# Optimization experiments

Measured on AMD Instinct MI355X. Metric: run time of the kernel, lower is better.

Reference implementation:

```python
import jax, jax.numpy as jnp
import numpy as np

N_HEAD = 4
EPS = 1e-5

def _layernorm(x, g, b):
    mu = jnp.mean(x, axis=-1, keepdims=True)
    var = jnp.mean(jnp.square(x - mu), axis=-1, keepdims=True)
    return (x - mu) * jax.lax.rsqrt(var + EPS) * g + b

def setup_inputs() -> dict:
    key = jax.random.key(0)
    ks = jax.random.split(key, 16)
    B, T, F = 8, 1024, 256
    dk = F // N_HEAD
    s = 1.0 / np.sqrt(F)
    return {
        "x": jax.random.normal(ks[0], (B, T, F), jnp.float32),
        "q_in": jax.random.normal(ks[1], (B, T, F), jnp.float32),
        "pos_k": jax.random.normal(ks[2], (T, T, dk), jnp.float32),
        "mask": jax.random.randint(ks[3], (B, T, T), 0, 2, jnp.int32),
        "ln_g": jnp.ones((F,), jnp.float32),
        "ln_b": jnp.zeros((F,), jnp.float32),
        "Wq": jax.random.normal(ks[4], (F, F), jnp.float32) * s,
        "bq": jnp.zeros((F,), jnp.float32),
        "Wk": jax.random.normal(ks[5], (F, F), jnp.float32) * s,
        "bk": jnp.zeros((F,), jnp.float32),
        "Wv": jax.random.normal(ks[6], (F, F), jnp.float32) * s,
        "bv": jnp.zeros((F,), jnp.float32),
        "Wo": jax.random.normal(ks[7], (F, F), jnp.float32) * s,
        "bo": jnp.zeros((F,), jnp.float32),
    }

def reference(x, q_in, pos_k, mask, ln_g, ln_b, Wq, bq, Wk, bk, Wv, bv, Wo, bo):
    B, T2, F = x.shape
    T1 = q_in.shape[1]
    h = N_HEAD
    dk = F // h
    xn = _layernorm(x, ln_g, ln_b)
    # (B, T, h, dk) -> (B, h, T, dk)
    q = (q_in @ Wq + bq).reshape(B, T1, h, dk).transpose(0, 2, 1, 3)
    k = (xn @ Wk + bk).reshape(B, T2, h, dk).transpose(0, 2, 1, 3)
    v = (xn @ Wv + bv).reshape(B, T2, h, dk).transpose(0, 2, 1, 3)
    A = jnp.einsum('bhqd,bhkd->bhqk', q, k)
    # relative position bias: B[b,h,q,t] = sum_d q[b,h,q,d] * pos_k[q,t,d]
    Bmat = jnp.einsum('bhqd,qtd->bhqt', q, pos_k)
    scores = (A + Bmat) / np.sqrt(dk)
    m = (mask[:, None, :, :] == 0)  # (B,1,T1,T2)
    min_val = jnp.finfo(scores.dtype).min
    scores = jnp.where(m, min_val, scores)
    attn = jax.nn.softmax(scores, axis=-1)
    attn = jnp.where(m, 0.0, attn)
    out = jnp.einsum('bhqk,bhkd->bhqd', attn, v)
    out = out.transpose(0, 2, 1, 3).reshape(B, T1, F)
    return out @ Wo + bo
```

## Files before the change

### kernel.cpp

```cpp
#include <hip/hip_runtime.h>
#include <hip/hip_bf16.h>

#define TT 1024
#define FF 256

typedef float  f4v  __attribute__((ext_vector_type(4)));
typedef float  f16v __attribute__((ext_vector_type(16)));
typedef __bf16 bf8v __attribute__((ext_vector_type(8)));
typedef unsigned short us8v __attribute__((ext_vector_type(8)));
typedef unsigned short us4v __attribute__((ext_vector_type(4)));

static __device__ __forceinline__ unsigned short f2bf(float x) {
    return __builtin_bit_cast(unsigned short, (__bf16)x);
}
static __device__ __forceinline__ float bf2f(unsigned short u) {
    return (float)__builtin_bit_cast(__bf16, u);
}
static __device__ __forceinline__ bf8v us2bf(us8v v) {
    return __builtin_bit_cast(bf8v, v);
}

__global__ __launch_bounds__(256) void k_wprep(
    const float* __restrict__ Wq, const float* __restrict__ Wk,
    const float* __restrict__ Wv, const float* __restrict__ Wo,
    unsigned short* __restrict__ Wt)
{
    __shared__ unsigned short T[32][36];
    const float* W = (blockIdx.y == 0) ? Wq : (blockIdx.y == 1) ? Wk
                   : (blockIdx.y == 2) ? Wv : Wo;
    unsigned short* dst = Wt + (blockIdx.y << 16);
    const int kt = (blockIdx.x >> 3) << 5, nt = (blockIdx.x & 7) << 5;
    const int r = threadIdx.x >> 3, c0 = (threadIdx.x & 7) << 2;
    const f4v w = *(const f4v*)&W[(kt + r) * FF + nt + c0];
    #pragma unroll
    for (int j = 0; j < 4; ++j) T[c0 + j][r] = f2bf(w[j]);
    __syncthreads();
    *(us4v*)&dst[(nt + r) * FF + kt + c0] = *(const us4v*)&T[r][c0];
}

__global__ __launch_bounds__(256) void k_ln(
    const float* __restrict__ x, const float* __restrict__ qin,
    const float* __restrict__ lng, const float* __restrict__ lnb,
    unsigned short* __restrict__ xn_bf, unsigned short* __restrict__ qin_bf)
{
    const int tid = threadIdx.x, lane = tid & 63, wv = tid >> 6;
    const int r0 = blockIdx.x << 4;

    #pragma unroll
    for (int u = 0; u < 4; ++u) {
        const int i4 = ((u << 8) + tid) << 2;
        const int r = i4 >> 8, c = i4 & 255;
        const f4v qv = *(const f4v*)&qin[(r0 + r) * FF + c];
        us4v o;
        #pragma unroll
        for (int j = 0; j < 4; ++j) o[j] = f2bf(qv[j]);
        *(us4v*)&qin_bf[(r0 + r) * FF + c] = o;
    }

    #pragma unroll
    for (int rr = 0; rr < 4; ++rr) {
        const int row = r0 + (wv << 2) + rr;
        float v[4], s = 0.f, s2 = 0.f;
        #pragma unroll
        for (int c4 = 0; c4 < 4; ++c4) {
            v[c4] = x[row * FF + (c4 << 6) + lane];
            s += v[c4]; s2 += v[c4] * v[c4];
        }
        #pragma unroll
        for (int off = 1; off < 64; off <<= 1) {
            s  += __shfl_xor(s, off);
            s2 += __shfl_xor(s2, off);
        }
        const float mu  = s * (1.f / FF);
        const float rsd = rsqrtf(s2 * (1.f / FF) - mu * mu + 1e-5f);
        #pragma unroll
        for (int c4 = 0; c4 < 4; ++c4) {
            const int c = (c4 << 6) + lane;
            xn_bf[row * FF + c] = f2bf((v[c4] - mu) * rsd * lng[c] + lnb[c]);
        }
    }
}

__global__ __launch_bounds__(256) void k_proj(
    const unsigned short* __restrict__ qin_bf, const unsigned short* __restrict__ xn_bf,
    const unsigned short* __restrict__ Wt,
    const float* __restrict__ bq, const float* __restrict__ bk, const float* __restrict__ bv,
    unsigned short* __restrict__ Qh, unsigned short* __restrict__ Kh,
    unsigned short* __restrict__ Vt)
{
    __shared__ __align__(16) unsigned short As[64 * 264];
    const int z = blockIdx.y;
    const unsigned short* A = (z == 0) ? qin_bf : xn_bf;
    const unsigned short* W = Wt + (z << 16);
    const float* bias = (z == 0) ? bq : (z == 1) ? bk : bv;
    unsigned short* dst = (z == 0) ? Qh : (z == 1) ? Kh : Vt;
    const int tid = threadIdx.x;
    const int m0 = blockIdx.x << 6;

    #pragma unroll
    for (int u = 0; u < 8; ++u) {
        const int idx = (u << 8) + tid;
        const int r = idx >> 5, c = (idx & 31) << 3;
        *(us8v*)&As[r * 264 + c] = *(const us8v*)&A[(m0 + r) * FF + c];
    }
    __syncthreads();

    const int lane = tid & 63, nw = tid >> 6, gq = lane >> 5, l31 = lane & 31;
    f16v acc[2][2];
    #pragma unroll
    for (int i = 0; i < 2; ++i)
        #pragma unroll
        for (int j = 0; j < 2; ++j)
            #pragma unroll
            for (int e = 0; e < 16; ++e) acc[i][j][e] = 0.f;

    for (int ks = 0; ks < 16; ++ks) {
        const int k0 = (ks << 4) + (gq << 3);
        bf8v af[2], wf[2];
        af[0] = us2bf(*(const us8v*)&As[l31 * 264 + k0]);
        af[1] = us2bf(*(const us8v*)&As[(32 + l31) * 264 + k0]);
        wf[0] = us2bf(*(const us8v*)&W[((nw << 6) + l31) * FF + k0]);
        wf[1] = us2bf(*(const us8v*)&W[((nw << 6) + 32 + l31) * FF + k0]);
        if (z == 2) {
            #pragma unroll
            for (int ti = 0; ti < 2; ++ti)
                #pragma unroll
                for (int tj = 0; tj < 2; ++tj)
                    acc[ti][tj] = __builtin_amdgcn_mfma_f32_32x32x16_bf16(
                        wf[tj], af[ti], acc[ti][tj], 0, 0, 0);
        } else {
            #pragma unroll
            for (int ti = 0; ti < 2; ++ti)
                #pragma unroll
                for (int tj = 0; tj < 2; ++tj)
                    acc[ti][tj] = __builtin_amdgcn_mfma_f32_32x32x16_bf16(
                        af[ti], wf[tj], acc[ti][tj], 0, 0, 0);
        }
    }

    if (z != 2) {
        #pragma unroll
        for (int ti = 0; ti < 2; ++ti)
            #pragma unroll
            for (int tj = 0; tj < 2; ++tj)
                #pragma unroll
                for (int reg = 0; reg < 16; ++reg) {
                    const int row = (reg & 3) + ((reg >> 2) << 3) + (gq << 2);
                    const int tg = m0 + (ti << 5) + row;
                    const int n = (nw << 6) + (tj << 5) + l31;
                    float val = acc[ti][tj][reg] + bias[n];
                    if (z == 0) val *= 0.125f;
                    const int b = tg >> 10, t = tg & 1023;
                    dst[(((b << 2) + nw) << 16) + (t << 6) + (tj << 5) + l31] = f2bf(val);
                }
    } else {
        #pragma unroll
        for (int ti = 0; ti < 2; ++ti)
            #pragma unroll
            for (int tj = 0; tj < 2; ++tj)
                #pragma unroll
                for (int reg = 0; reg < 16; ++reg) {
                    const int row = (reg & 3) + ((reg >> 2) << 3) + (gq << 2);
                    const int d = (tj << 5) + row;
                    const int tg = m0 + (ti << 5) + l31;
                    const float val = acc[ti][tj][reg] + bias[(nw << 6) + d];
                    const int b = tg >> 10, t = tg & 1023;
                    dst[(((b << 2) + nw) << 16) + (d << 10) + t] = f2bf(val);
                }
    }
}

__global__ __launch_bounds__(256) void k_bterm(
    const unsigned short* __restrict__ Qh, const float* __restrict__ posk,
    const int* __restrict__ mask, unsigned short* __restrict__ Bm, int qbase)
{
    const int tid = threadIdx.x, lane = tid & 63, wv = tid >> 6;
    const int gq = lane >> 5, m = lane & 31;
    const int ql = blockIdx.y, q = qbase + ql;

    bf8v afr[4];
    #pragma unroll
    for (int kk = 0; kk < 4; ++kk)
        afr[kk] = us2bf(*(const us8v*)&Qh[(m << 16) + (q << 6) + (kk << 4) + (gq << 3)]);

    const int t0w = (blockIdx.x << 9) + (wv << 7);
    for (int st = 0; st < 4; ++st) {
        const int t = t0w + (st << 5) + m;
        bf8v bfr[4];
        #pragma unroll
        for (int kk = 0; kk < 4; ++kk) {
            const int d0 = (kk << 4) + (gq << 3);
            const f4v p0 = *(const f4v*)&posk[(((q << 10) + t) << 6) + d0];
            const f4v p1 = *(const f4v*)&posk[(((q << 10) + t) << 6) + d0 + 4];
            bf8v bb;
            bb[0] = (__bf16)p0[0]; bb[1] = (__bf16)p0[1];
            bb[2] = (__bf16)p0[2]; bb[3] = (__bf16)p0[3];
            bb[4] = (__bf16)p1[0]; bb[5] = (__bf16)p1[1];
            bb[6] = (__bf16)p1[2]; bb[7] = (__bf16)p1[3];
            bfr[kk] = bb;
        }
        f16v acc;
        #pragma unroll
        for (int i = 0; i < 16; ++i) acc[i] = 0.f;
        #pragma unroll
        for (int kk = 0; kk < 4; ++kk)
            acc = __builtin_amdgcn_mfma_f32_32x32x16_bf16(afr[kk], bfr[kk], acc, 0, 0, 0);

        int mk[4];
        #pragma unroll
        for (int g = 0; g < 4; ++g)
            mk[g] = mask[(((g << 1) + gq) << 20) + (q << 10) + t];
        #pragma unroll
        for (int reg = 0; reg < 16; ++reg) {
            const int g = reg >> 2;
            const int bhr = (reg & 3) + (g << 3) + (gq << 2);
            const float val = mk[g] ? acc[reg] : -3.0e38f;
            Bm[(bhr << 19) + (ql << 10) + t] = f2bf(val);
        }
    }
}

__global__ __launch_bounds__(256) void k_attn(
    const unsigned short* __restrict__ Qh, const unsigned short* __restrict__ Kh,
    const unsigned short* __restrict__ Vt, const unsigned short* __restrict__ Bm,
    unsigned short* __restrict__ aout_bf, int qbase)
{
    __shared__ __align__(16) unsigned short Qs[32 * 72];
    __shared__ __align__(16) unsigned short Ps[32 * 136];
    __shared__ __align__(16) unsigned short Bs[32 * 136];
    __shared__ float m_s[32], l_s[32], wmax[4][32], wsum[4][32];

    const int tid = threadIdx.x, lane = tid & 63, wv = tid >> 6;
    const int l15 = lane & 15, quad = lane >> 4;
    const int bh = blockIdx.x & 31, qt = blockIdx.x >> 5;
    const int b = bh >> 2, h = bh & 3;
    const int q0l = qt << 5, q0g = qbase + q0l;

    if (tid < 32) { m_s[tid] = -3.0e38f; l_s[tid] = 0.f; }
    {
        const int r = tid >> 3, d0 = (tid & 7) << 3;
        *(us8v*)&Qs[r * 72 + d0] =
            *(const us8v*)&Qh[(bh << 16) + ((q0g + r) << 6) + d0];
    }

    f4v o0, o1;
    #pragma unroll
    for (int i = 0; i < 4; ++i) { o0[i] = 0.f; o1[i] = 0.f; }

    for (int it = 0; it < 8; ++it) {
        const int t0 = it << 7;
        #pragma unroll
        for (int u = 0; u < 2; ++u) {
            const int idx = (u << 8) + tid;
            const int r = idx >> 4, c = (idx & 15) << 3;
            *(us8v*)&Bs[r * 136 + c] =
                *(const us8v*)&Bm[(bh << 19) + ((q0l + r) << 10) + t0 + c];
        }
        __syncthreads();

        f4v s00, s01, s10, s11;
        #pragma unroll
        for (int i = 0; i < 4; ++i) { s00[i]=0.f; s01[i]=0.f; s10[i]=0.f; s11[i]=0.f; }
        #pragma unroll
        for (int kk = 0; kk < 2; ++kk) {
            const int d0 = (kk << 5) + (quad << 3);
            const bf8v aq0 = us2bf(*(const us8v*)&Qs[l15 * 72 + d0]);
            const bf8v aq1 = us2bf(*(const us8v*)&Qs[(16 + l15) * 72 + d0]);
            const bf8v kb0 = us2bf(*(const us8v*)&Kh[(bh << 16) + ((t0 + (wv << 5) + l15) << 6) + d0]);
            const bf8v kb1 = us2bf(*(const us8v*)&Kh[(bh << 16) + ((t0 + (wv << 5) + 16 + l15) << 6) + d0]);
            s00 = __builtin_amdgcn_mfma_f32_16x16x32_bf16(aq0, kb0, s00, 0, 0, 0);
            s01 = __builtin_amdgcn_mfma_f32_16x16x32_bf16(aq0, kb1, s01, 0, 0, 0);
            s10 = __builtin_amdgcn_mfma_f32_16x16x32_bf16(aq1, kb0, s10, 0, 0, 0);
            s11 = __builtin_amdgcn_mfma_f32_16x16x32_bf16(aq1, kb1, s11, 0, 0, 0);
        }

        float sv[2][2][4];
        #pragma unroll
        for (int mf = 0; mf < 2; ++mf)
            #pragma unroll
            for (int nf = 0; nf < 2; ++nf) {
                const f4v sfr = (mf == 0) ? (nf == 0 ? s00 : s01)
                                          : (nf == 0 ? s10 : s11);
                const int tl = (wv << 5) + (nf << 4) + l15;
                #pragma unroll
                for (int r = 0; r < 4; ++r) {
                    const int q = (mf << 4) + (quad << 2) + r;
                    sv[mf][nf][r] = sfr[r] + bf2f(Bs[q * 136 + tl]);
                }
            }

        float rmax[2][4];
        #pragma unroll
        for (int mf = 0; mf < 2; ++mf)
            #pragma unroll
            for (int r = 0; r < 4; ++r) {
                float vx = fmaxf(sv[mf][0][r], sv[mf][1][r]);
                vx = fmaxf(vx, __shfl_xor(vx, 1));
                vx = fmaxf(vx, __shfl_xor(vx, 2));
                vx = fmaxf(vx, __shfl_xor(vx, 4));
                vx = fmaxf(vx, __shfl_xor(vx, 8));
                rmax[mf][r] = vx;
            }
        if (l15 == 0) {
            #pragma unroll
            for (int mf = 0; mf < 2; ++mf)
                #pragma unroll
                for (int r = 0; r < 4; ++r)
                    wmax[wv][(mf << 4) + (quad << 2) + r] = rmax[mf][r];
        }
        __syncthreads();

        float alpha[2][4], mnew[2][4];
        #pragma unroll
        for (int mf = 0; mf < 2; ++mf)
            #pragma unroll
            for (int r = 0; r < 4; ++r) {
                const int q = (mf << 4) + (quad << 2) + r;
                const float tm = fmaxf(fmaxf(wmax[0][q], wmax[1][q]),
                                       fmaxf(wmax[2][q], wmax[3][q]));
                const float mo = m_s[q];
                const float mn = fmaxf(mo, tm);
                mnew[mf][r]  = mn;
                alpha[mf][r] = __expf(mo - mn);
            }
        #pragma unroll
        for (int mf = 0; mf < 2; ++mf)
            #pragma unroll
            for (int r = 0; r < 4; ++r) {
                const int q = (mf << 4) + (quad << 2) + r;
                const float p0 = __expf(sv[mf][0][r] - mnew[mf][r]);
                const float p1 = __expf(sv[mf][1][r] - mnew[mf][r]);
                Ps[q * 136 + (wv << 5) + l15]      = f2bf(p0);
                Ps[q * 136 + (wv << 5) + 16 + l15] = f2bf(p1);
                float rs2 = p0 + p1;
                rs2 += __shfl_xor(rs2, 1);
                rs2 += __shfl_xor(rs2, 2);
                rs2 += __shfl_xor(rs2, 4);
                rs2 += __shfl_xor(rs2, 8);
                if (l15 == 0) wsum[wv][q] = rs2;
            }
        #pragma unroll
        for (int r = 0; r < 4; ++r) { o0[r] *= alpha[0][r]; o1[r] *= alpha[1][r]; }
        __syncthreads();

        if (tid < 32) {
            const int q = tid;
            const float tm = fmaxf(fmaxf(wmax[0][q], wmax[1][q]),
                                   fmaxf(wmax[2][q], wmax[3][q]));
            const float mo = m_s[q];
            const float mn = fmaxf(mo, tm);
            l_s[q] = l_s[q] * __expf(mo - mn)
                   + (wsum[0][q] + wsum[1][q]) + (wsum[2][q] + wsum[3][q]);
            m_s[q] = mn;
        }

        #pragma unroll
        for (int kk = 0; kk < 4; ++kk) {
            const int toff = (kk << 5) + (quad << 3);
            const bf8v vbf = us2bf(*(const us8v*)&Vt[(bh << 16) + (((wv << 4) + l15) << 10) + t0 + toff]);
            const bf8v ap0 = us2bf(*(const us8v*)&Ps[l15 * 136 + toff]);
            const bf8v ap1 = us2bf(*(const us8v*)&Ps[(16 + l15) * 136 + toff]);
            o0 = __builtin_amdgcn_mfma_f32_16x16x32_bf16(ap0, vbf, o0, 0, 0, 0);
            o1 = __builtin_amdgcn_mfma_f32_16x16x32_bf16(ap1, vbf, o1, 0, 0, 0);
        }
    }
    __syncthreads();

    const int d = (wv << 4) + l15;
    #pragma unroll
    for (int mf = 0; mf < 2; ++mf)
        #pragma unroll
        for (int r = 0; r < 4; ++r) {
            const int q = (mf << 4) + (quad << 2) + r;
            const float ov = ((mf == 0) ? o0[r] : o1[r]) / l_s[q];
            aout_bf[((b << 10) + q0g + q) * FF + (h << 6) + d] = f2bf(ov);
        }
}

__global__ __launch_bounds__(256) void k_oproj(
    const unsigned short* __restrict__ aout_bf, const unsigned short* __restrict__ Wot,
    const float* __restrict__ bo, float* __restrict__ out)
{
    __shared__ __align__(16) unsigned short As[64 * 264];
    const int tid = threadIdx.x;
    const int m0 = blockIdx.x << 6;

    #pragma unroll
    for (int u = 0; u < 8; ++u) {
        const int idx = (u << 8) + tid;
        const int r = idx >> 5, c = (idx & 31) << 3;
        *(us8v*)&As[r * 264 + c] = *(const us8v*)&aout_bf[(m0 + r) * FF + c];
    }
    __syncthreads();

    const int lane = tid & 63, nw = tid >> 6, gq = lane >> 5, l31 = lane & 31;
    f16v acc[2][2];
    #pragma unroll
    for (int i = 0; i < 2; ++i)
        #pragma unroll
        for (int j = 0; j < 2; ++j)
            #pragma unroll
            for (int e = 0; e < 16; ++e) acc[i][j][e] = 0.f;

    for (int ks = 0; ks < 16; ++ks) {
        const int k0 = (ks << 4) + (gq << 3);
        bf8v af[2], wf[2];
        af[0] = us2bf(*(const us8v*)&As[l31 * 264 + k0]);
        af[1] = us2bf(*(const us8v*)&As[(32 + l31) * 264 + k0]);
        wf[0] = us2bf(*(const us8v*)&Wot[((nw << 6) + l31) * FF + k0]);
        wf[1] = us2bf(*(const us8v*)&Wot[((nw << 6) + 32 + l31) * FF + k0]);
        #pragma unroll
        for (int ti = 0; ti < 2; ++ti)
            #pragma unroll
            for (int tj = 0; tj < 2; ++tj)
                acc[ti][tj] = __builtin_amdgcn_mfma_f32_32x32x16_bf16(
                    af[ti], wf[tj], acc[ti][tj], 0, 0, 0);
    }

    #pragma unroll
    for (int ti = 0; ti < 2; ++ti)
        #pragma unroll
        for (int tj = 0; tj < 2; ++tj)
            #pragma unroll
            for (int reg = 0; reg < 16; ++reg) {
                const int row = (reg & 3) + ((reg >> 2) << 3) + (gq << 2);
                const int tg = m0 + (ti << 5) + row;
                const int n = (nw << 6) + (tj << 5) + l31;
                out[tg * FF + n] = acc[ti][tj][reg] + bo[n];
            }
}

extern "C" void kernel_launch(void* const* d_in, const int* in_sizes, int n_in,
                              void* d_out, int out_size, void* d_ws, size_t ws_size,
                              hipStream_t stream)
{
    const float* x    = (const float*)d_in[0];
    const float* qin  = (const float*)d_in[1];
    const float* posk = (const float*)d_in[2];
    const int*   mask = (const int*)d_in[3];
    const float* ln_g = (const float*)d_in[4];
    const float* ln_b = (const float*)d_in[5];
    const float* Wq   = (const float*)d_in[6];
    const float* bq   = (const float*)d_in[7];
    const float* Wk   = (const float*)d_in[8];
    const float* bk   = (const float*)d_in[9];
    const float* Wv   = (const float*)d_in[10];
    const float* bv   = (const float*)d_in[11];
    const float* Wo   = (const float*)d_in[12];
    const float* bo   = (const float*)d_in[13];
    float* out = (float*)d_out;

    char* ws = (char*)d_ws;
    unsigned short* wWt   = (unsigned short*)(ws);
    unsigned short* qinb  = (unsigned short*)(ws + (size_t)(1u << 20));
    unsigned short* xnb   = (unsigned short*)(ws + (size_t)(5u << 20));
    unsigned short* Qh    = (unsigned short*)(ws + (size_t)(9u << 20));
    unsigned short* Kh    = (unsigned short*)(ws + (size_t)(13u << 20));
    unsigned short* Vth   = (unsigned short*)(ws + (size_t)(17u << 20));
    unsigned short* aoutb = (unsigned short*)(ws + (size_t)(21u << 20));
    unsigned short* Bm    = (unsigned short*)(ws + (size_t)(25u << 20));

    hipLaunchKernelGGL(k_wprep, dim3(64, 4), dim3(256), 0, stream, Wq, Wk, Wv, Wo, wWt);
    hipLaunchKernelGGL(k_ln, dim3(512), dim3(256), 0, stream,
                       x, qin, ln_g, ln_b, xnb, qinb);
    hipLaunchKernelGGL(k_proj, dim3(128, 3), dim3(256), 0, stream,
                       qinb, xnb, wWt, bq, bk, bv, Qh, Kh, Vth);
    for (int half = 0; half < 2; ++half) {
        const int qbase = half * 512;
        hipLaunchKernelGGL(k_bterm, dim3(2, 512), dim3(256), 0, stream,
                           Qh, posk, mask, Bm, qbase);
        hipLaunchKernelGGL(k_attn, dim3(512), dim3(256), 0, stream,
                           Qh, Kh, Vth, Bm, aoutb, qbase);
    }
    hipLaunchKernelGGL(k_oproj, dim3(128), dim3(256), 0, stream,
                       aoutb, wWt + (3 << 16), bo, out);
}
```

Before: 536.3 us.

## Merge bterm/attn halves, double-buffer bias tiles, keep softmax stats in registers

Removes the two-half loop so k_bterm and k_attn each launch once over all 1024 queries, with the Bm buffer doubled to hold full rows. k_bterm now handles one 32-wide t tile per wave with more blocks instead of looping. k_attn prefetches the next bias tile into registers and a second LDS buffer during compute, keeps running max/sum in per-thread registers instead of shared arrays, remaps blockIdx to bh, and sets occupancy launch bounds. The cost is double the Bm workspace (now reaching 25MB+64MB) and higher register pressure.

```diff
diff --git a/kernel.cpp b/kernel.cpp
--- a/kernel.cpp
+++ b/kernel.cpp
@@ -172,91 +172,118 @@
 
 __global__ __launch_bounds__(256) void k_bterm(
     const unsigned short* __restrict__ Qh, const float* __restrict__ posk,
-    const int* __restrict__ mask, unsigned short* __restrict__ Bm, int qbase)
+    const int* __restrict__ mask, unsigned short* __restrict__ Bm)
 {
     const int tid = threadIdx.x, lane = tid & 63, wv = tid >> 6;
     const int gq = lane >> 5, m = lane & 31;
-    const int ql = blockIdx.y, q = qbase + ql;
+    const int q = blockIdx.y;
+    const int t = (blockIdx.x << 7) + (wv << 5) + m;
 
     bf8v afr[4];
     #pragma unroll
     for (int kk = 0; kk < 4; ++kk)
         afr[kk] = us2bf(*(const us8v*)&Qh[(m << 16) + (q << 6) + (kk << 4) + (gq << 3)]);
 
-    const int t0w = (blockIdx.x << 9) + (wv << 7);
-    for (int st = 0; st < 4; ++st) {
-        const int t = t0w + (st << 5) + m;
-        bf8v bfr[4];
-        #pragma unroll
-        for (int kk = 0; kk < 4; ++kk) {
-            const int d0 = (kk << 4) + (gq << 3);
-            const f4v p0 = *(const f4v*)&posk[(((q << 10) + t) << 6) + d0];
-            const f4v p1 = *(const f4v*)&posk[(((q << 10) + t) << 6) + d0 + 4];
-            bf8v bb;
-            bb[0] = (__bf16)p0[0]; bb[1] = (__bf16)p0[1];
-            bb[2] = (__bf16)p0[2]; bb[3] = (__bf16)p0[3];
-            bb[4] = (__bf16)p1[0]; bb[5] = (__bf16)p1[1];
-            bb[6] = (__bf16)p1[2]; bb[7] = (__bf16)p1[3];
-            bfr[kk] = bb;
-        }
-        f16v acc;
-        #pragma unroll
-        for (int i = 0; i < 16; ++i) acc[i] = 0.f;
-        #pragma unroll
-        for (int kk = 0; kk < 4; ++kk)
-            acc = __builtin_amdgcn_mfma_f32_32x32x16_bf16(afr[kk], bfr[kk], acc, 0, 0, 0);
-
-        int mk[4];
-        #pragma unroll
-        for (int g = 0; g < 4; ++g)
-            mk[g] = mask[(((g << 1) + gq) << 20) + (q << 10) + t];
-        #pragma unroll
-        for (int reg = 0; reg < 16; ++reg) {
-            const int g = reg >> 2;
-            const int bhr = (reg & 3) + (g << 3) + (gq << 2);
-            const float val = mk[g] ? acc[reg] : -3.0e38f;
-            Bm[(bhr << 19) + (ql << 10) + t] = f2bf(val);
-        }
-    }
-}
-
-__global__ __launch_bounds__(256) void k_attn(
+    bf8v bfr[4];
+    #pragma unroll
+    for (int kk = 0; kk < 4; ++kk) {
+        const int d0 = (kk << 4) + (gq << 3);
+        const f4v p0 = *(const f4v*)&posk[(((q << 10) + t) << 6) + d0];
+        const f4v p1 = *(const f4v*)&posk[(((q << 10) + t) << 6) + d0 + 4];
+        bf8v bb;
+        bb[0] = (__bf16)p0[0]; bb[1] = (__bf16)p0[1];
+        bb[2] = (__bf16)p0[2]; bb[3] = (__bf16)p0[3];
+        bb[4] = (__bf16)p1[0]; bb[5] = (__bf16)p1[1];
+        bb[6] = (__bf16)p1[2]; bb[7] = (__bf16)p1[3];
+        bfr[kk] = bb;
+    }
+
+    f16v acc;
+    #pragma unroll
+    for (int i = 0; i < 16; ++i) acc[i] = 0.f;
+    #pragma unroll
+    for (int kk = 0; kk < 4; ++kk)
+        acc = __builtin_amdgcn_mfma_f32_32x32x16_bf16(afr[kk], bfr[kk], acc, 0, 0, 0);
+
+    int mk[4];
+    #pragma unroll
+    for (int g = 0; g < 4; ++g)
+        mk[g] = mask[(((g << 1) + gq) << 20) + (q << 10) + t];
+    #pragma unroll
+    for (int reg = 0; reg < 16; ++reg) {
+        const int g = reg >> 2;
+        const int bhr = (reg & 3) + (g << 3) + (gq << 2);
+        const float val = mk[g] ? acc[reg] : -3.0e38f;
+        Bm[(bhr << 20) + (q << 10) + t] = f2bf(val);
+    }
+}
+
+__global__ __launch_bounds__(256, 4) void k_attn(
     const unsigned short* __restrict__ Qh, const unsigned short* __restrict__ Kh,
     const unsigned short* __restrict__ Vt, const unsigned short* __restrict__ Bm,
-    unsigned short* __restrict__ aout_bf, int qbase)
+    unsigned short* __restrict__ aout_bf)
 {
     __shared__ __align__(16) unsigned short Qs[32 * 72];
     __shared__ __align__(16) unsigned short Ps[32 * 136];
-    __shared__ __align__(16) unsigned short Bs[32 * 136];
-    __shared__ float m_s[32], l_s[32], wmax[4][32], wsum[4][32];
+    __shared__ __align__(16) unsigned short Bs[2][32 * 136];
+    __shared__ float wmax[4][32], wsum[4][32];
 
     const int tid = threadIdx.x, lane = tid & 63, wv = tid >> 6;
     const int l15 = lane & 15, quad = lane >> 4;
-    const int bh = blockIdx.x & 31, qt = blockIdx.x >> 5;
+    const int blk = blockIdx.x;
+    const int bh = ((blk & 7) << 2) | ((blk >> 3) & 3);
+    const int qt = blk >> 5;
     const int b = bh >> 2, h = bh & 3;
-    const int q0l = qt << 5, q0g = qbase + q0l;
-
-    if (tid < 32) { m_s[tid] = -3.0e38f; l_s[tid] = 0.f; }
+    const int q0 = qt << 5;
+
     {
         const int r = tid >> 3, d0 = (tid & 7) << 3;
         *(us8v*)&Qs[r * 72 + d0] =
-            *(const us8v*)&Qh[(bh << 16) + ((q0g + r) << 6) + d0];
-    }
-
-    f4v o0, o1;
-    #pragma unroll
-    for (int i = 0; i < 4; ++i) { o0[i] = 0.f; o1[i] = 0.f; }
-
-    for (int it = 0; it < 8; ++it) {
-        const int t0 = it << 7;
+            *(const us8v*)&Qh[(bh << 16) + ((q0 + r) << 6) + d0];
+    }
+    {
         #pragma unroll
         for (int u = 0; u < 2; ++u) {
             const int idx = (u << 8) + tid;
             const int r = idx >> 4, c = (idx & 15) << 3;
-            *(us8v*)&Bs[r * 136 + c] =
-                *(const us8v*)&Bm[(bh << 19) + ((q0l + r) << 10) + t0 + c];
-        }
-        __syncthreads();
+            *(us8v*)&Bs[0][r * 136 + c] =
+                *(const us8v*)&Bm[(bh << 20) + ((q0 + r) << 10) + c];
+        }
+    }
+    __syncthreads();
+
+    f4v o0, o1;
+    float mreg[2][4], lreg[2][4], alpha[2][4];
+    #pragma unroll
+    for (int i = 0; i < 4; ++i) { o0[i] = 0.f; o1[i] = 0.f; }
+    #pragma unroll
+    for (int mf = 0; mf < 2; ++mf)
+        #pragma unroll
+        for (int r = 0; r < 4; ++r) { mreg[mf][r] = -3.0e38f; lreg[mf][r] = 0.f; }
+
+    for (int it = 0; it < 8; ++it) {
+        const int t0 = it << 7;
+        const int cur = it & 1;
+
+        us8v pf[2];
+        if (it < 7) {
+            #pragma unroll
+            for (int u = 0; u < 2; ++u) {
+                const int idx = (u << 8) + tid;
+                const int r = idx >> 4, c = (idx & 15) << 3;
+                pf[u] = *(const us8v*)&Bm[(bh << 20) + ((q0 + r) << 10) + t0 + 128 + c];
+            }
+        }
+
+        if (it > 0) {
+            #pragma unroll
+            for (int mf = 0; mf < 2; ++mf)
+                #pragma unroll
+                for (int r = 0; r < 4; ++r) {
+                    const int q = (mf << 4) + (quad << 2) + r;
+                    lreg[mf][r] += (wsum[0][q] + wsum[1][q]) + (wsum[2][q] + wsum[3][q]);
+                }
+        }
 
         f4v s00, s01, s10, s11;
         #pragma unroll
@@ -285,11 +312,10 @@
                 #pragma unroll
                 for (int r = 0; r < 4; ++r) {
                     const int q = (mf << 4) + (quad << 2) + r;
-                    sv[mf][nf][r] = sfr[r] + bf2f(Bs[q * 136 + tl]);
+                    sv[mf][nf][r] = sfr[r] + bf2f(Bs[cur][q * 136 + tl]);
                 }
             }
 
-        float rmax[2][4];
         #pragma unroll
         for (int mf = 0; mf < 2; ++mf)
             #pragma unroll
@@ -299,18 +325,18 @@
                 vx = fmaxf(vx, __shfl_xor(vx, 2));
                 vx = fmaxf(vx, __shfl_xor(vx, 4));
                 vx = fmaxf(vx, __shfl_xor(vx, 8));
-                rmax[mf][r] = vx;
-            }
-        if (l15 == 0) {
-            #pragma unroll
-            for (int mf = 0; mf < 2; ++mf)
-                #pragma unroll
-                for (int r = 0; r < 4; ++r)
-                    wmax[wv][(mf << 4) + (quad << 2) + r] = rmax[mf][r];
+                if (l15 == 0) wmax[wv][(mf << 4) + (quad << 2) + r] = vx;
+            }
+        if (it < 7) {
+            #pragma unroll
+            for (int u = 0; u < 2; ++u) {
+                const int idx = (u << 8) + tid;
+                const int r = idx >> 4, c = (idx & 15) << 3;
+                *(us8v*)&Bs[cur ^ 1][r * 136 + c] = pf[u];
+            }
         }
         __syncthreads();
 
-        float alpha[2][4], mnew[2][4];
         #pragma unroll
         for (int mf = 0; mf < 2; ++mf)
             #pragma unroll
@@ -318,18 +344,18 @@
                 const int q = (mf << 4) + (quad << 2) + r;
                 const float tm = fmaxf(fmaxf(wmax[0][q], wmax[1][q]),
                                        fmaxf(wmax[2][q], wmax[3][q]));
-                const float mo = m_s[q];
+                const float mo = mreg[mf][r];
                 const float mn = fmaxf(mo, tm);
-                mnew[mf][r]  = mn;
                 alpha[mf][r] = __expf(mo - mn);
+                mreg[mf][r] = mn;
             }
         #pragma unroll
         for (int mf = 0; mf < 2; ++mf)
             #pragma unroll
             for (int r = 0; r < 4; ++r) {
                 const int q = (mf << 4) + (quad << 2) + r;
-                const float p0 = __expf(sv[mf][0][r] - mnew[mf][r]);
-                const float p1 = __expf(sv[mf][1][r] - mnew[mf][r]);
+                const float p0 = __expf(sv[mf][0][r] - mreg[mf][r]);
+                const float p1 = __expf(sv[mf][1][r] - mreg[mf][r]);
                 Ps[q * 136 + (wv << 5) + l15]      = f2bf(p0);
                 Ps[q * 136 + (wv << 5) + 16 + l15] = f2bf(p1);
                 float rs2 = p0 + p1;
@@ -341,18 +367,11 @@
             }
         #pragma unroll
         for (int r = 0; r < 4; ++r) { o0[r] *= alpha[0][r]; o1[r] *= alpha[1][r]; }
+        #pragma unroll
+        for (int mf = 0; mf < 2; ++mf)
+            #pragma unroll
+            for (int r = 0; r < 4; ++r) lreg[mf][r] *= alpha[mf][r];
         __syncthreads();
-
-        if (tid < 32) {
-            const int q = tid;
-            const float tm = fmaxf(fmaxf(wmax[0][q], wmax[1][q]),
-                                   fmaxf(wmax[2][q], wmax[3][q]));
-            const float mo = m_s[q];
-            const float mn = fmaxf(mo, tm);
-            l_s[q] = l_s[q] * __expf(mo - mn)
-                   + (wsum[0][q] + wsum[1][q]) + (wsum[2][q] + wsum[3][q]);
-            m_s[q] = mn;
-        }
 
         #pragma unroll
         for (int kk = 0; kk < 4; ++kk) {
@@ -364,16 +383,23 @@
             o1 = __builtin_amdgcn_mfma_f32_16x16x32_bf16(ap1, vbf, o1, 0, 0, 0);
         }
     }
-    __syncthreads();
-
-    const int d = (wv << 4) + l15;
+
     #pragma unroll
     for (int mf = 0; mf < 2; ++mf)
         #pragma unroll
         for (int r = 0; r < 4; ++r) {
             const int q = (mf << 4) + (quad << 2) + r;
-            const float ov = ((mf == 0) ? o0[r] : o1[r]) / l_s[q];
-            aout_bf[((b << 10) + q0g + q) * FF + (h << 6) + d] = f2bf(ov);
+            lreg[mf][r] += (wsum[0][q] + wsum[1][q]) + (wsum[2][q] + wsum[3][q]);
+        }
+
+    const int d = (wv << 4) + l15;
+    #pragma unroll
+    for (int mf = 0; mf < 2; ++mf)
+        #pragma unroll
+        for (int r = 0; r < 4; ++r) {
+            const int q = (mf << 4) + (quad << 2) + r;
+            const float ov = ((mf == 0) ? o0[r] : o1[r]) / lreg[mf][r];
+            aout_bf[((b << 10) + q0 + q) * FF + (h << 6) + d] = f2bf(ov);
         }
 }
 
@@ -465,13 +491,10 @@
                        x, qin, ln_g, ln_b, xnb, qinb);
     hipLaunchKernelGGL(k_proj, dim3(128, 3), dim3(256), 0, stream,
                        qinb, xnb, wWt, bq, bk, bv, Qh, Kh, Vth);
-    for (int half = 0; half < 2; ++half) {
-        const int qbase = half * 512;
-        hipLaunchKernelGGL(k_bterm, dim3(2, 512), dim3(256), 0, stream,
-                           Qh, posk, mask, Bm, qbase);
-        hipLaunchKernelGGL(k_attn, dim3(512), dim3(256), 0, stream,
-                           Qh, Kh, Vth, Bm, aoutb, qbase);
-    }
+    hipLaunchKernelGGL(k_bterm, dim3(8, 1024), dim3(256), 0, stream,
+                       Qh, posk, mask, Bm);
+    hipLaunchKernelGGL(k_attn, dim3(1024), dim3(256), 0, stream,
+                       Qh, Kh, Vth, Bm, aoutb);
     hipLaunchKernelGGL(k_oproj, dim3(128), dim3(256), 0, stream,
                        aoutb, wWt + (3 << 16), bo, out);
 }
```

After: 533.3 us. Within noise of the previous version (-0.6%).
